# Kernel optimization log

Hardware: AMD Instinct MI355X
Metric: run time of the kernel (lower is better)

The kernel has to match this reference:

```python
import jax, jax.numpy as jnp
import numpy as np

N = 100000
E = 1600000
F_IN = 64
H = 128
D_OUT = 1
G = 512  # number of graphs
EPS = 1e-5


def setup_inputs() -> dict:
    key = jax.random.key(0)
    ks = jax.random.split(key, 16)
    x = jax.random.normal(ks[0], (N, F_IN), dtype=jnp.float32)
    edge_index = jax.random.randint(ks[1], (2, E), 0, N, dtype=jnp.int64)
    batch = jnp.sort(jax.random.randint(ks[2], (N,), 0, G, dtype=jnp.int64))
    def lin(k, fin, fout):
        s = 1.0 / np.sqrt(fin)
        k1, k2 = jax.random.split(k)
        return (jax.random.uniform(k1, (fin, fout), jnp.float32, -s, s),
                jax.random.uniform(k2, (fout,), jnp.float32, -s, s))
    fc1_w, fc1_b = lin(ks[3], F_IN, H)
    gc1_w, gc1_b = lin(ks[4], H, H)
    gc2_w, gc2_b = lin(ks[5], H, H)
    fc2_w, fc2_b = lin(ks[6], H, D_OUT)
    gn1_g = jnp.ones((H,), jnp.float32); gn1_b = jnp.zeros((H,), jnp.float32)
    gn2_g = jnp.ones((H,), jnp.float32); gn2_b = jnp.zeros((H,), jnp.float32)
    return dict(x=x, edge_index=edge_index, batch=batch,
                fc1_w=fc1_w, fc1_b=fc1_b, gc1_w=gc1_w, gc1_b=gc1_b,
                gn1_g=gn1_g, gn1_b=gn1_b, gc2_w=gc2_w, gc2_b=gc2_b,
                gn2_g=gn2_g, gn2_b=gn2_b, fc2_w=fc2_w, fc2_b=fc2_b)


def gcn_conv(x, src, dst, deg_inv_sqrt, w, b):
    # x: [N,H]; symmetric-normalized aggregation with self-loops already in src/dst
    h = x @ w  # [N, H_out]
    norm = deg_inv_sqrt[src] * deg_inv_sqrt[dst]  # [E+N]
    msgs = h[src] * norm[:, None]
    out = jax.ops.segment_sum(msgs, dst, num_segments=N)
    return out + b


def graph_layernorm(x, batch, gamma, beta, counts):
    # PyG LayerNorm mode='graph': normalize over all nodes+channels per graph
    denom = jnp.maximum(counts * x.shape[1], 1.0)  # [G]
    mean = jax.ops.segment_sum(x.sum(-1), batch, num_segments=G) / denom
    xc = x - mean[batch][:, None]
    var = jax.ops.segment_sum((xc * xc).sum(-1), batch, num_segments=G) / denom
    inv = jax.lax.rsqrt(var + EPS)
    return xc * inv[batch][:, None] * gamma + beta


def reference(x, edge_index, batch, fc1_w, fc1_b, gc1_w, gc1_b, gn1_g, gn1_b,
              gc2_w, gc2_b, gn2_g, gn2_b, fc2_w, fc2_b):
    loops = jnp.arange(N, dtype=edge_index.dtype)
    src = jnp.concatenate([edge_index[0], loops])
    dst = jnp.concatenate([edge_index[1], loops])
    deg = jax.ops.segment_sum(jnp.ones_like(dst, dtype=x.dtype), dst, num_segments=N)
    deg_inv_sqrt = jnp.where(deg > 0, jax.lax.rsqrt(jnp.maximum(deg, 1.0)), 0.0)
    counts = jax.ops.segment_sum(jnp.ones_like(batch, dtype=x.dtype), batch, num_segments=G)

    hx = x @ fc1_w + fc1_b
    h = jax.nn.relu(graph_layernorm(gcn_conv(hx, src, dst, deg_inv_sqrt, gc1_w, gc1_b), batch, gn1_g, gn1_b, counts))
    h = jax.nn.relu(graph_layernorm(gcn_conv(h, src, dst, deg_inv_sqrt, gc2_w, gc2_b), batch, gn2_g, gn2_b, counts))
    pooled = jax.ops.segment_sum(h, batch, num_segments=G) / jnp.maximum(counts, 1.0)[:, None]
    return pooled @ fc2_w + fc2_b  # [G, D_OUT]
```

## Files before the change

kernel.cpp:

```cpp
#include <hip/hip_runtime.h>

#define NN 100000
#define EE 1600000
#define FIN 64
#define HH 128
#define GG 512
#define EPSV 1e-5f

__global__ void initk(int* deg, int* cursor, int* counts,
                      float* gsum1, float* gsq1, float* gsum2, float* gsq2,
                      float* pooled) {
  int i = blockIdx.x * 256 + threadIdx.x;
  if (i < NN) { deg[i] = 1; cursor[i] = 0; }
  if (i < GG) { counts[i] = 0; gsum1[i] = 0.f; gsq1[i] = 0.f; gsum2[i] = 0.f; gsq2[i] = 0.f; }
  if (i < GG * HH) pooled[i] = 0.f;
}

__global__ void countk(const int* __restrict__ ei, const int* __restrict__ batch,
                       int* deg, int* counts) {
  int i = blockIdx.x * 256 + threadIdx.x;
  if (i < EE) atomicAdd(&deg[ei[EE + i]], 1);
  if (i < NN) atomicAdd(&counts[batch[i]], 1);
}

__global__ void disk(const int* __restrict__ deg, float* __restrict__ dis) {
  int i = blockIdx.x * 256 + threadIdx.x;
  if (i < NN) dis[i] = rsqrtf((float)deg[i]);
}

#define SCHUNK 1024
__global__ void scan1(const int* __restrict__ deg, int* __restrict__ bsum) {
  __shared__ int red[256];
  int b = blockIdx.x, t = threadIdx.x;
  int base = b * SCHUNK + t * 4;
  int s = 0;
#pragma unroll
  for (int i = 0; i < 4; i++) { int idx = base + i; if (idx < NN) s += deg[idx] - 1; }
  red[t] = s; __syncthreads();
  for (int o = 128; o > 0; o >>= 1) { if (t < o) red[t] += red[t + o]; __syncthreads(); }
  if (t == 0) bsum[b] = red[0];
}

__global__ void scan2(const int* __restrict__ bsum, int* __restrict__ boff,
                      int* __restrict__ rowptr, int nblk) {
  if (threadIdx.x == 0 && blockIdx.x == 0) {
    int run = 0;
    for (int i = 0; i < nblk; i++) { boff[i] = run; run += bsum[i]; }
    rowptr[NN] = run;
  }
}

__global__ void scan3(const int* __restrict__ deg, const int* __restrict__ boff,
                      int* __restrict__ rowptr) {
  __shared__ int sc[2][256];
  int b = blockIdx.x, t = threadIdx.x;
  int base = b * SCHUNK + t * 4;
  int v[4]; int s = 0;
#pragma unroll
  for (int i = 0; i < 4; i++) {
    int idx = base + i;
    v[i] = (idx < NN) ? (deg[idx] - 1) : 0;
    s += v[i];
  }
  int pp = 0;
  sc[0][t] = s; __syncthreads();
  for (int o = 1; o < 256; o <<= 1) {
    int val = sc[pp][t];
    if (t >= o) val += sc[pp][t - o];
    sc[pp ^ 1][t] = val; __syncthreads();
    pp ^= 1;
  }
  int excl = sc[pp][t] - s;
  int p = boff[b] + excl;
#pragma unroll
  for (int i = 0; i < 4; i++) {
    int idx = base + i;
    if (idx < NN) rowptr[idx] = p;
    p += v[i];
  }
}

__global__ void scatterk(const int* __restrict__ ei, int* cursor,
                         const int* __restrict__ rowptr, int* __restrict__ colsrc) {
  int e = blockIdx.x * 256 + threadIdx.x;
  if (e >= EE) return;
  int d = ei[EE + e];
  int pos = rowptr[d] + atomicAdd(&cursor[d], 1);
  colsrc[pos] = ei[e];
}

__global__ void gemm64(const float* __restrict__ X, const float* __restrict__ W,
                       const float* __restrict__ bias, float* __restrict__ Y) {
  __shared__ float xs[8 * 64];
  int n0 = blockIdx.x * 8, t = threadIdx.x;
  const float* xb = X + (size_t)n0 * 64;
  for (int i = t; i < 512; i += 128) xs[i] = xb[i];
  __syncthreads();
  float bv = bias[t];
  float acc[8];
#pragma unroll
  for (int n = 0; n < 8; n++) acc[n] = bv;
#pragma unroll 4
  for (int k = 0; k < 64; k++) {
    float wv = W[k * 128 + t];
#pragma unroll
    for (int n = 0; n < 8; n++) acc[n] = fmaf(xs[n * 64 + k], wv, acc[n]);
  }
#pragma unroll
  for (int n = 0; n < 8; n++) Y[(size_t)(n0 + n) * 128 + t] = acc[n];
}

template <bool LN>
__global__ void gemm128(const float* __restrict__ X, const float* __restrict__ W,
                        float* __restrict__ Y,
                        const int* __restrict__ batch,
                        const float* __restrict__ mean, const float* __restrict__ inv,
                        const float* __restrict__ gamma, const float* __restrict__ beta) {
  __shared__ float xs[8 * 128];
  int n0 = blockIdx.x * 8, t = threadIdx.x;
  const float* xb = X + (size_t)n0 * 128;
  if (LN) {
#pragma unroll
    for (int j = 0; j < 8; j++) {
      int node = n0 + j;
      int bb = batch[node];
      float v = xb[j * 128 + t];
      v = (v - mean[bb]) * inv[bb] * gamma[t] + beta[t];
      xs[j * 128 + t] = fmaxf(v, 0.f);
    }
  } else {
    for (int i = t; i < 1024; i += 128) xs[i] = xb[i];
  }
  __syncthreads();
  float acc[8];
#pragma unroll
  for (int n = 0; n < 8; n++) acc[n] = 0.f;
#pragma unroll 4
  for (int k = 0; k < 128; k++) {
    float wv = W[k * 128 + t];
#pragma unroll
    for (int n = 0; n < 8; n++) acc[n] = fmaf(xs[n * 128 + k], wv, acc[n]);
  }
#pragma unroll
  for (int n = 0; n < 8; n++) Y[(size_t)(n0 + n) * 128 + t] = acc[n];
}

__global__ __launch_bounds__(256, 8)
void aggk(const float* __restrict__ Hin, const int* __restrict__ colsrc,
          const int* __restrict__ rowptr, const float* __restrict__ dis,
          const float* __restrict__ bias, const int* __restrict__ batch,
          float* __restrict__ Yout, float* __restrict__ gsum, float* __restrict__ gsq) {
  int wid = threadIdx.x >> 6;
  int n = blockIdx.x * 4 + wid;
  int lane = threadIdx.x & 63;
  int half = lane >> 5, q = lane & 31;
  float di = dis[n];
  int rp0 = rowptr[n];
  int m = rowptr[n + 1] - rp0 + 1;
  float4 acc = make_float4(0.f, 0.f, 0.f, 0.f);
  int p = 0;
  for (; p + 7 < m; p += 8) {
    int s[4]; float w[4]; float4 h[4];
#pragma unroll
    for (int j = 0; j < 4; j++) {
      int idx = p + 2 * j + half;
      s[j] = (idx == m - 1) ? n : colsrc[rp0 + idx];
    }
#pragma unroll
    for (int j = 0; j < 4; j++) {
      w[j] = dis[s[j]] * di;
      h[j] = *reinterpret_cast<const float4*>(&Hin[(size_t)s[j] * HH + q * 4]);
    }
#pragma unroll
    for (int j = 0; j < 4; j++) {
      acc.x = fmaf(h[j].x, w[j], acc.x);
      acc.y = fmaf(h[j].y, w[j], acc.y);
      acc.z = fmaf(h[j].z, w[j], acc.z);
      acc.w = fmaf(h[j].w, w[j], acc.w);
    }
  }
  for (; p < m; p += 2) {
    int idx = p + half;
    if (idx < m) {
      int s = (idx == m - 1) ? n : colsrc[rp0 + idx];
      float w = dis[s] * di;
      float4 h = *reinterpret_cast<const float4*>(&Hin[(size_t)s * HH + q * 4]);
      acc.x = fmaf(h.x, w, acc.x);
      acc.y = fmaf(h.y, w, acc.y);
      acc.z = fmaf(h.z, w, acc.z);
      acc.w = fmaf(h.w, w, acc.w);
    }
  }
  acc.x += __shfl_xor(acc.x, 32);
  acc.y += __shfl_xor(acc.y, 32);
  acc.z += __shfl_xor(acc.z, 32);
  acc.w += __shfl_xor(acc.w, 32);
  float4 bv = *reinterpret_cast<const float4*>(&bias[q * 4]);
  acc.x += bv.x; acc.y += bv.y; acc.z += bv.z; acc.w += bv.w;
  if (half == 0) {
    *reinterpret_cast<float4*>(&Yout[(size_t)n * HH + q * 4]) = acc;
  }
  float s1 = acc.x + acc.y + acc.z + acc.w;
  float s2 = acc.x * acc.x + acc.y * acc.y + acc.z * acc.z + acc.w * acc.w;
  for (int o = 16; o > 0; o >>= 1) {
    s1 += __shfl_down(s1, o);
    s2 += __shfl_down(s2, o);
  }
  if (lane == 0) {
    int b = batch[n];
    atomicAdd(&gsum[b], s1);
    atomicAdd(&gsq[b], s2);
  }
}

__global__ void lnfinal(const float* __restrict__ gsum, const float* __restrict__ gsq,
                        const int* __restrict__ counts,
                        float* __restrict__ mean, float* __restrict__ inv) {
  int g = blockIdx.x * 256 + threadIdx.x;
  if (g >= GG) return;
  float denom = fmaxf((float)counts[g] * (float)HH, 1.f);
  float m = gsum[g] / denom;
  float v = gsq[g] / denom - m * m;
  mean[g] = m;
  inv[g] = rsqrtf(fmaxf(v, 0.f) + EPSV);
}

__global__ void poolk(const float* __restrict__ A, const int* __restrict__ batch,
                      const float* __restrict__ mean, const float* __restrict__ inv,
                      const float* __restrict__ gamma, const float* __restrict__ beta,
                      float* __restrict__ pooled) {
  int idx = blockIdx.x * 256 + threadIdx.x;
  if (idx >= NN * HH) return;
  int n = idx >> 7, ch = idx & 127;
  int b = batch[n];
  float v = (A[idx] - mean[b]) * inv[b] * gamma[ch] + beta[ch];
  v = fmaxf(v, 0.f);
  atomicAdd(&pooled[b * 128 + ch], v);
}

__global__ void finalk(const float* __restrict__ pooled, const int* __restrict__ counts,
                       const float* __restrict__ w, const float* __restrict__ b,
                       float* __restrict__ out) {
  int g = blockIdx.x, t = threadIdx.x;
  float cnt = fmaxf((float)counts[g], 1.f);
  float v = pooled[g * 128 + t] / cnt * w[t];
  for (int o = 32; o > 0; o >>= 1) v += __shfl_down(v, o);
  __shared__ float l[2];
  if ((t & 63) == 0) l[t >> 6] = v;
  __syncthreads();
  if (t == 0) out[g] = l[0] + l[1] + b[0];
}

extern "C" void kernel_launch(void* const* d_in, const int* in_sizes, int n_in,
                              void* d_out, int out_size, void* d_ws, size_t ws_size,
                              hipStream_t stream) {
  const float* x = (const float*)d_in[0];
  const int* ei = (const int*)d_in[1];
  const int* batch = (const int*)d_in[2];
  const float* fc1_w = (const float*)d_in[3];
  const float* fc1_b = (const float*)d_in[4];
  const float* gc1_w = (const float*)d_in[5];
  const float* gc1_b = (const float*)d_in[6];
  const float* gn1_g = (const float*)d_in[7];
  const float* gn1_b = (const float*)d_in[8];
  const float* gc2_w = (const float*)d_in[9];
  const float* gc2_b = (const float*)d_in[10];
  const float* gn2_g = (const float*)d_in[11];
  const float* gn2_b = (const float*)d_in[12];
  const float* fc2_w = (const float*)d_in[13];
  const float* fc2_b = (const float*)d_in[14];
  float* out = (float*)d_out;

  char* p = (char*)d_ws;
  auto alloc = [&](size_t bytes) { void* r = (void*)p; p += ((bytes + 255) / 256) * 256; return r; };
  float* A = (float*)alloc((size_t)NN * HH * 4);
  float* B = (float*)alloc((size_t)NN * HH * 4);
  int* colsrc = (int*)alloc((size_t)EE * 4);
  int* rowptr = (int*)alloc((size_t)(NN + 1) * 4);
  int* deg = (int*)alloc((size_t)NN * 4);
  int* cursor = (int*)alloc((size_t)NN * 4);
  float* dis = (float*)alloc((size_t)NN * 4);
  int* counts = (int*)alloc((size_t)GG * 4);
  float* gsum1 = (float*)alloc((size_t)GG * 4);
  float* gsq1 = (float*)alloc((size_t)GG * 4);
  float* gsum2 = (float*)alloc((size_t)GG * 4);
  float* gsq2 = (float*)alloc((size_t)GG * 4);
  float* mean1 = (float*)alloc((size_t)GG * 4);
  float* inv1 = (float*)alloc((size_t)GG * 4);
  float* mean2 = (float*)alloc((size_t)GG * 4);
  float* inv2 = (float*)alloc((size_t)GG * 4);
  float* pooled = (float*)alloc((size_t)GG * HH * 4);
  int* bsum = (int*)alloc(1024);
  int* boff = (int*)alloc(1024);

  int nblk = (NN + SCHUNK - 1) / SCHUNK;

  initk<<<(NN + 255) / 256, 256, 0, stream>>>(deg, cursor, counts, gsum1, gsq1, gsum2, gsq2, pooled);
  countk<<<(EE + 255) / 256, 256, 0, stream>>>(ei, batch, deg, counts);
  disk<<<(NN + 255) / 256, 256, 0, stream>>>(deg, dis);
  scan1<<<nblk, 256, 0, stream>>>(deg, bsum);
  scan2<<<1, 64, 0, stream>>>(bsum, boff, rowptr, nblk);
  scan3<<<nblk, 256, 0, stream>>>(deg, boff, rowptr);
  scatterk<<<(EE + 255) / 256, 256, 0, stream>>>(ei, cursor, rowptr, colsrc);

  gemm64<<<NN / 8, 128, 0, stream>>>(x, fc1_w, fc1_b, A);
  gemm128<false><<<NN / 8, 128, 0, stream>>>(A, gc1_w, B, nullptr, nullptr, nullptr, nullptr, nullptr);
  aggk<<<NN / 4, 256, 0, stream>>>(B, colsrc, rowptr, dis, gc1_b, batch, A, gsum1, gsq1);
  lnfinal<<<(GG + 255) / 256, 256, 0, stream>>>(gsum1, gsq1, counts, mean1, inv1);
  gemm128<true><<<NN / 8, 128, 0, stream>>>(A, gc2_w, B, batch, mean1, inv1, gn1_g, gn1_b);
  aggk<<<NN / 4, 256, 0, stream>>>(B, colsrc, rowptr, dis, gc2_b, batch, A, gsum2, gsq2);
  lnfinal<<<(GG + 255) / 256, 256, 0, stream>>>(gsum2, gsq2, counts, mean2, inv2);
  poolk<<<(NN * HH + 255) / 256, 256, 0, stream>>>(A, batch, mean2, inv2, gn2_g, gn2_b, pooled);
  finalk<<<GG, 128, 0, stream>>>(pooled, counts, fc2_w, fc2_b, out);
}
```

Baseline: 1.094 ms.

## Fold fc1 into gc1 weights and aggregate raw 64-wide features first

Precomputes Wp = fc1_w @ gc1_w and c1 = fc1_b @ gc1_w. Layer one now aggregates the raw 64-channel input over the graph first, then applies one 64x128 GEMM plus a rowsum*c1 bias term. That GEMM also produces the per-graph layernorm sums. This halves the gather width of the first aggregation and removes one full GEMM pass and an N x 128 round trip. It also software-prefetches the next edge indices in the gather loops. The cost is a small extra weight-prep kernel and a different floating-point summation order.

```diff
diff --git a/kernel.cpp b/kernel.cpp
--- a/kernel.cpp
+++ b/kernel.cpp
@@ -89,25 +89,131 @@
   colsrc[pos] = ei[e];
 }
 
-__global__ void gemm64(const float* __restrict__ X, const float* __restrict__ W,
-                       const float* __restrict__ bias, float* __restrict__ Y) {
-  __shared__ float xs[8 * 64];
+__global__ void prepw(const float* __restrict__ fc1w, const float* __restrict__ fc1b,
+                      const float* __restrict__ gc1w,
+                      float* __restrict__ Wp, float* __restrict__ c1) {
+  int k = blockIdx.x, t = threadIdx.x;
+  if (k < 64) {
+    float s = 0.f;
+    for (int j = 0; j < 128; j++) s = fmaf(fc1w[k * 128 + j], gc1w[j * 128 + t], s);
+    Wp[k * 128 + t] = s;
+  } else {
+    float s = 0.f;
+    for (int j = 0; j < 128; j++) s = fmaf(fc1b[j], gc1w[j * 128 + t], s);
+    c1[t] = s;
+  }
+}
+
+__global__ __launch_bounds__(256, 8)
+void aggx(const float* __restrict__ X, const int* __restrict__ colsrc,
+          const int* __restrict__ rowptr, const float* __restrict__ dis,
+          float* __restrict__ Y, float* __restrict__ rowsum) {
+  int wid = threadIdx.x >> 6;
+  int n = blockIdx.x * 4 + wid;
+  int lane = threadIdx.x & 63;
+  int slot = lane >> 4, q = lane & 15;
+  float di = dis[n];
+  int rp0 = rowptr[n];
+  int m = rowptr[n + 1] - rp0 + 1;
+  float4 acc = make_float4(0.f, 0.f, 0.f, 0.f);
+  float wsum = 0.f;
+  int s[4];
+#pragma unroll
+  for (int j = 0; j < 4; j++) {
+    int idx = 4 * j + slot;
+    s[j] = (idx >= m - 1) ? n : colsrc[rp0 + idx];
+  }
+  int p = 0;
+  for (; p + 15 < m; p += 16) {
+    int sn[4];
+#pragma unroll
+    for (int j = 0; j < 4; j++) {
+      int idx = p + 16 + 4 * j + slot;
+      sn[j] = (idx >= m - 1) ? n : colsrc[rp0 + idx];
+    }
+    float w[4]; float4 h[4];
+#pragma unroll
+    for (int j = 0; j < 4; j++) {
+      w[j] = dis[s[j]] * di;
+      h[j] = *reinterpret_cast<const float4*>(&X[(size_t)s[j] * FIN + q * 4]);
+    }
+#pragma unroll
+    for (int j = 0; j < 4; j++) {
+      acc.x = fmaf(h[j].x, w[j], acc.x);
+      acc.y = fmaf(h[j].y, w[j], acc.y);
+      acc.z = fmaf(h[j].z, w[j], acc.z);
+      acc.w = fmaf(h[j].w, w[j], acc.w);
+      wsum += w[j];
+    }
+#pragma unroll
+    for (int j = 0; j < 4; j++) s[j] = sn[j];
+  }
+  for (; p < m; p += 4) {
+    int idx = p + slot;
+    if (idx < m) {
+      int sv = (idx == m - 1) ? n : colsrc[rp0 + idx];
+      float w = dis[sv] * di;
+      float4 h = *reinterpret_cast<const float4*>(&X[(size_t)sv * FIN + q * 4]);
+      acc.x = fmaf(h.x, w, acc.x);
+      acc.y = fmaf(h.y, w, acc.y);
+      acc.z = fmaf(h.z, w, acc.z);
+      acc.w = fmaf(h.w, w, acc.w);
+      wsum += w;
+    }
+  }
+  acc.x += __shfl_xor(acc.x, 16); acc.y += __shfl_xor(acc.y, 16);
+  acc.z += __shfl_xor(acc.z, 16); acc.w += __shfl_xor(acc.w, 16);
+  wsum  += __shfl_xor(wsum, 16);
+  acc.x += __shfl_xor(acc.x, 32); acc.y += __shfl_xor(acc.y, 32);
+  acc.z += __shfl_xor(acc.z, 32); acc.w += __shfl_xor(acc.w, 32);
+  wsum  += __shfl_xor(wsum, 32);
+  if (slot == 0) {
+    *reinterpret_cast<float4*>(&Y[(size_t)n * FIN + q * 4]) = acc;
+  }
+  if (lane == 0) rowsum[n] = wsum;
+}
+
+__global__ void gemmA(const float* __restrict__ Y, const float* __restrict__ Wp,
+                      const float* __restrict__ c1, const float* __restrict__ gc1b,
+                      const float* __restrict__ rowsum, const int* __restrict__ batch,
+                      float* __restrict__ A, float* __restrict__ gsum, float* __restrict__ gsq) {
+  __shared__ float ys[8 * 64];
+  __shared__ float l1[8][2], l2[8][2];
   int n0 = blockIdx.x * 8, t = threadIdx.x;
-  const float* xb = X + (size_t)n0 * 64;
-  for (int i = t; i < 512; i += 128) xs[i] = xb[i];
+  reinterpret_cast<float4*>(ys)[t] =
+      reinterpret_cast<const float4*>(Y + (size_t)n0 * 64)[t];
   __syncthreads();
-  float bv = bias[t];
+  float cv = c1[t], bv = gc1b[t];
   float acc[8];
 #pragma unroll
   for (int n = 0; n < 8; n++) acc[n] = bv;
 #pragma unroll 4
   for (int k = 0; k < 64; k++) {
-    float wv = W[k * 128 + t];
-#pragma unroll
-    for (int n = 0; n < 8; n++) acc[n] = fmaf(xs[n * 64 + k], wv, acc[n]);
-  }
-#pragma unroll
-  for (int n = 0; n < 8; n++) Y[(size_t)(n0 + n) * 128 + t] = acc[n];
+    float wv = Wp[k * 128 + t];
+#pragma unroll
+    for (int n = 0; n < 8; n++) acc[n] = fmaf(ys[n * 64 + k], wv, acc[n]);
+  }
+#pragma unroll
+  for (int n = 0; n < 8; n++) {
+    acc[n] = fmaf(rowsum[n0 + n], cv, acc[n]);
+    A[(size_t)(n0 + n) * 128 + t] = acc[n];
+  }
+  int wid = t >> 6, lane = t & 63;
+#pragma unroll
+  for (int n = 0; n < 8; n++) {
+    float s1v = acc[n], s2v = acc[n] * acc[n];
+    for (int o = 32; o > 0; o >>= 1) {
+      s1v += __shfl_down(s1v, o);
+      s2v += __shfl_down(s2v, o);
+    }
+    if (lane == 0) { l1[n][wid] = s1v; l2[n][wid] = s2v; }
+  }
+  __syncthreads();
+  if (t < 8) {
+    int b = batch[n0 + t];
+    atomicAdd(&gsum[b], l1[t][0] + l1[t][1]);
+    atomicAdd(&gsq[b], l2[t][0] + l2[t][1]);
+  }
 }
 
 template <bool LN>
@@ -158,14 +264,21 @@
   int rp0 = rowptr[n];
   int m = rowptr[n + 1] - rp0 + 1;
   float4 acc = make_float4(0.f, 0.f, 0.f, 0.f);
+  int s[4];
+#pragma unroll
+  for (int j = 0; j < 4; j++) {
+    int idx = 2 * j + half;
+    s[j] = (idx >= m - 1) ? n : colsrc[rp0 + idx];
+  }
   int p = 0;
   for (; p + 7 < m; p += 8) {
-    int s[4]; float w[4]; float4 h[4];
-#pragma unroll
-    for (int j = 0; j < 4; j++) {
-      int idx = p + 2 * j + half;
-      s[j] = (idx == m - 1) ? n : colsrc[rp0 + idx];
-    }
+    int sn[4];
+#pragma unroll
+    for (int j = 0; j < 4; j++) {
+      int idx = p + 8 + 2 * j + half;
+      sn[j] = (idx >= m - 1) ? n : colsrc[rp0 + idx];
+    }
+    float w[4]; float4 h[4];
 #pragma unroll
     for (int j = 0; j < 4; j++) {
       w[j] = dis[s[j]] * di;
@@ -178,13 +291,15 @@
       acc.z = fmaf(h[j].z, w[j], acc.z);
       acc.w = fmaf(h[j].w, w[j], acc.w);
     }
+#pragma unroll
+    for (int j = 0; j < 4; j++) s[j] = sn[j];
   }
   for (; p < m; p += 2) {
     int idx = p + half;
     if (idx < m) {
-      int s = (idx == m - 1) ? n : colsrc[rp0 + idx];
-      float w = dis[s] * di;
-      float4 h = *reinterpret_cast<const float4*>(&Hin[(size_t)s * HH + q * 4]);
+      int sv = (idx == m - 1) ? n : colsrc[rp0 + idx];
+      float w = dis[sv] * di;
+      float4 h = *reinterpret_cast<const float4*>(&Hin[(size_t)sv * HH + q * 4]);
       acc.x = fmaf(h.x, w, acc.x);
       acc.y = fmaf(h.y, w, acc.y);
       acc.z = fmaf(h.z, w, acc.z);
@@ -275,11 +390,13 @@
   auto alloc = [&](size_t bytes) { void* r = (void*)p; p += ((bytes + 255) / 256) * 256; return r; };
   float* A = (float*)alloc((size_t)NN * HH * 4);
   float* B = (float*)alloc((size_t)NN * HH * 4);
+  float* Yx = B;
   int* colsrc = (int*)alloc((size_t)EE * 4);
   int* rowptr = (int*)alloc((size_t)(NN + 1) * 4);
   int* deg = (int*)alloc((size_t)NN * 4);
   int* cursor = (int*)alloc((size_t)NN * 4);
   float* dis = (float*)alloc((size_t)NN * 4);
+  float* rowsum = (float*)alloc((size_t)NN * 4);
   int* counts = (int*)alloc((size_t)GG * 4);
   float* gsum1 = (float*)alloc((size_t)GG * 4);
   float* gsq1 = (float*)alloc((size_t)GG * 4);
@@ -290,6 +407,8 @@
   float* mean2 = (float*)alloc((size_t)GG * 4);
   float* inv2 = (float*)alloc((size_t)GG * 4);
   float* pooled = (float*)alloc((size_t)GG * HH * 4);
+  float* Wp = (float*)alloc((size_t)64 * 128 * 4);
+  float* c1 = (float*)alloc((size_t)128 * 4);
   int* bsum = (int*)alloc(1024);
   int* boff = (int*)alloc(1024);
 
@@ -302,10 +421,10 @@
   scan2<<<1, 64, 0, stream>>>(bsum, boff, rowptr, nblk);
   scan3<<<nblk, 256, 0, stream>>>(deg, boff, rowptr);
   scatterk<<<(EE + 255) / 256, 256, 0, stream>>>(ei, cursor, rowptr, colsrc);
-
-  gemm64<<<NN / 8, 128, 0, stream>>>(x, fc1_w, fc1_b, A);
-  gemm128<false><<<NN / 8, 128, 0, stream>>>(A, gc1_w, B, nullptr, nullptr, nullptr, nullptr, nullptr);
-  aggk<<<NN / 4, 256, 0, stream>>>(B, colsrc, rowptr, dis, gc1_b, batch, A, gsum1, gsq1);
+  prepw<<<65, 128, 0, stream>>>(fc1_w, fc1_b, gc1_w, Wp, c1);
+
+  aggx<<<NN / 4, 256, 0, stream>>>(x, colsrc, rowptr, dis, Yx, rowsum);
+  gemmA<<<NN / 8, 128, 0, stream>>>(Yx, Wp, c1, gc1_b, rowsum, batch, A, gsum1, gsq1);
   lnfinal<<<(GG + 255) / 256, 256, 0, stream>>>(gsum1, gsq1, counts, mean1, inv1);
   gemm128<true><<<NN / 8, 128, 0, stream>>>(A, gc2_w, B, batch, mean1, inv1, gn1_g, gn1_b);
   aggk<<<NN / 4, 256, 0, stream>>>(B, colsrc, rowptr, dis, gc2_b, batch, A, gsum2, gsq2);
```

After: 1.040 ms. 5.0% less time.
